# Kernel tuning notes

Measured on AMD Instinct MI355X. Metric: run time of the kernel, lower is better.

Reference implementation:

```python
import jax, jax.numpy as jnp
import numpy as np

KP_EXTENT = 1.2  # matches init_kwargs KP_extent


def setup_inputs() -> dict:
    key = jax.random.key(0)
    k1, k2, k3, k4, k5, k6 = jax.random.split(key, 6)
    N, M, H, K, CIN, COUT = 50000, 50000, 40, 15, 64, 128
    q_pts = jax.random.normal(k1, (N, 3), dtype=jnp.float32)
    s_pts = jax.random.normal(k2, (M, 3), dtype=jnp.float32)
    # indices in [0, M]; index M hits the padded shadow point / zero feature row
    neighb_inds = jax.random.randint(k3, (N, H), 0, M + 1)
    x = jax.random.normal(k4, (M, CIN), dtype=jnp.float32)
    # kernel point disposition in a sphere of given radius (values arbitrary for math check)
    kernel_points = jax.random.normal(k5, (K, 3), dtype=jnp.float32)
    weights = jax.random.normal(k6, (K, CIN, COUT), dtype=jnp.float32) * 0.05
    return {"q_pts": q_pts, "s_pts": s_pts, "neighb_inds": neighb_inds,
            "x": x, "kernel_points": kernel_points, "weights": weights}


def reference(q_pts, s_pts, neighb_inds, x, kernel_points, weights):
    # pad support points with a far-away shadow point (index M)
    shadow = jnp.full((1, s_pts.shape[1]), 1.0e6, dtype=s_pts.dtype)
    s_pad = jnp.concatenate([s_pts, shadow], axis=0)          # [M+1, 3]
    neighbors = s_pad[neighb_inds] - q_pts[:, None, :]        # [N, H, 3]

    # squared distances to kernel points via |n|^2 + |k|^2 - 2 n.k (avoids [N,H,K,3] tensor)
    n2 = jnp.sum(neighbors * neighbors, axis=-1)              # [N, H]
    k2 = jnp.sum(kernel_points * kernel_points, axis=-1)      # [K]
    cross = jnp.einsum('nhd,kd->nhk', neighbors, kernel_points)
    sq_distances = jnp.maximum(n2[:, :, None] + k2[None, None, :] - 2.0 * cross, 0.0)  # [N, H, K]

    # linear KP influence
    all_weights = jnp.clip(1.0 - jnp.sqrt(sq_distances) / KP_EXTENT, 0.0)  # [N, H, K]

    # pad features with a zero row for shadow neighbors
    x_pad = jnp.concatenate([x, jnp.zeros((1, x.shape[1]), dtype=x.dtype)], axis=0)  # [M+1, C]
    neighb_x = x_pad[neighb_inds]                             # [N, H, C]

    # weighted aggregation per kernel point, then per-kernel-point matmul and sum
    weighted_features = jnp.einsum('nhk,nhc->nkc', all_weights, neighb_x)  # [N, K, Cin]
    output_features = jnp.einsum('nkc,kco->no', weighted_features, weights)  # [N, Cout]

    # normalize by number of valid neighbors (feature-sum > 0 heuristic, as in source)
    neighbor_features_sum = jnp.sum(neighb_x, axis=-1)        # [N, H]
    neighbor_num = jnp.maximum(jnp.sum(neighbor_features_sum > 0.0, axis=-1), 1)  # [N]
    return output_features / neighbor_num[:, None].astype(output_features.dtype)
```

## Files before the change

kernel.cpp:

```cpp
#include <hip/hip_runtime.h>
#include <math.h>

typedef unsigned short ushort_t;
typedef __attribute__((ext_vector_type(8))) short bf16x8;
typedef __attribute__((ext_vector_type(4))) float f32x4;

constexpr int H    = 40;
constexpr int KKP  = 15;
constexpr int CIN  = 64;
constexpr int COUT = 128;
constexpr int QB   = 32;
constexpr int NT   = 512;
constexpr int NP   = QB * H;
constexpr int SWF  = 968;
constexpr int SWT  = 2056;
constexpr int CSTR = 48;
constexpr float INV_KPE = 1.0f / 1.2f;

constexpr int OFF_CIND = 61952;
constexpr int OFF_QCNT = 65152;
constexpr int OFF_CNT  = 65280;
constexpr int LDS_TOT  = 65408;
static_assert(LDS_TOT <= 65536, "LDS over 64KB static limit");

__device__ __forceinline__ ushort_t f2bf(float f) {
    union { float f; unsigned u; } v; v.f = f;
    unsigned r = v.u + 0x7FFFu + ((v.u >> 16) & 1u);
    return (ushort_t)(r >> 16);
}
__device__ __forceinline__ unsigned pk2(ushort_t a, ushort_t b) {
    return (unsigned)a | ((unsigned)b << 16);
}

__global__ __launch_bounds__(256) void prep_kernel(const float* __restrict__ x,
                                                   float* __restrict__ rowsum,
                                                   ushort_t* __restrict__ xb,
                                                   int M, int write_xb) {
    int row  = blockIdx.x * 4 + (threadIdx.x >> 6);
    int lane = threadIdx.x & 63;
    if (row >= M) return;
    float v = x[row * CIN + lane];
    if (write_xb) xb[row * CIN + lane] = f2bf(v);
    #pragma unroll
    for (int off = 32; off > 0; off >>= 1) v += __shfl_down(v, off, 64);
    if (lane == 0) rowsum[row] = v;
}

__global__ __launch_bounds__(256) void wprep_kernel(const float* __restrict__ wmat,
                                                    ushort_t* __restrict__ wb) {
    int t = blockIdx.x * 256 + threadIdx.x;
    if (t >= 30 * 8 * 64) return;
    int lane = t & 63;
    int ot   = (t >> 6) & 7;
    int jt   = t >> 9;
    int o  = ot * 16 + (lane & 15);
    int kb = jt * 32 + (lane >> 4) * 8;
    unsigned pk[4];
    #pragma unroll
    for (int r = 0; r < 4; ++r) {
        unsigned lo = f2bf(wmat[(kb + 2 * r) * COUT + o]);
        unsigned hi = f2bf(wmat[(kb + 2 * r + 1) * COUT + o]);
        pk[r] = lo | (hi << 16);
    }
    *(uint4*)&wb[(size_t)t * 8] = make_uint4(pk[0], pk[1], pk[2], pk[3]);
}

template<bool BF16X>
__global__ __launch_bounds__(NT, 4) void kpconv_main(
    const float* __restrict__ q_pts, const float* __restrict__ s_pts,
    const int*   __restrict__ nbinds, const float* __restrict__ xf,
    const ushort_t* __restrict__ xb,  const float* __restrict__ kp,
    const ushort_t* __restrict__ wb,  const float* __restrict__ rowsum,
    float* __restrict__ out, int N, int M)
{
    __shared__ __align__(16) unsigned char smem[LDS_TOT];
    ushort_t* const wT   = (ushort_t*)smem;
    ushort_t* const WF16 = (ushort_t*)smem;
    ushort_t* const cind = (ushort_t*)(smem + OFF_CIND);
    int* const qcnt = (int*)(smem + OFF_QCNT);
    int* const cnt  = (int*)(smem + OFF_CNT);

    const int tid = threadIdx.x;
    const int q0  = blockIdx.x * QB;

    for (int i = tid; i < 3855; i += NT)
        ((uint4*)wT)[i] = make_uint4(0, 0, 0, 0);
    if (tid < 200) ((uint4*)cind)[tid] = make_uint4(0, 0, 0, 0);
    if (tid < QB) { qcnt[tid] = 0; cnt[tid] = 0; }
    __syncthreads();

    for (int p = tid; p < NP; p += NT) {
        int q  = p / H;
        int h  = p - q * H;
        int gq  = q0 + q;
        int gqc = min(gq, N - 1);
        int ind = nbinds[gqc * H + h];
        bool shadow = (ind >= M);
        float nx = 0.f, ny = 0.f, nz = 0.f;
        if (!shadow) {
            nx = s_pts[ind * 3 + 0] - q_pts[gqc * 3 + 0];
            ny = s_pts[ind * 3 + 1] - q_pts[gqc * 3 + 1];
            nz = s_pts[ind * 3 + 2] - q_pts[gqc * 3 + 2];
            if (rowsum[ind] > 0.0f) atomicAdd(&cnt[q], 1);
        }
        float n2 = nx * nx + ny * ny + nz * nz;
        float w[KKP];
        float wmax = 0.f;
        #pragma unroll
        for (int k = 0; k < KKP; ++k) {
            float wv = 0.f;
            if (!shadow) {
                float kx = kp[k * 3 + 0], ky = kp[k * 3 + 1], kz = kp[k * 3 + 2];
                float k2 = kx * kx + ky * ky + kz * kz;
                float cross = nx * kx + ny * ky + nz * kz;
                float sq = fmaxf(n2 + k2 - 2.0f * cross, 0.0f);
                wv = fmaxf(1.0f - sqrtf(sq) * INV_KPE, 0.0f);
            }
            w[k] = wv;
            wmax = fmaxf(wmax, wv);
        }
        if (wmax > 0.f) {
            int slot = atomicAdd(&qcnt[q], 1);
            cind[q * CSTR + slot] = (ushort_t)ind;
            #pragma unroll
            for (int k = 0; k < KKP; ++k)
                wT[k * SWT + q * 64 + slot] = f2bf(w[k]);
        }
    }
    __syncthreads();

    const int wid  = tid >> 6;
    const int lane = tid & 63;
    const int l15  = lane & 15;
    const int kg   = lane >> 4;
    const int cg   = wid & 3;
    const int qh2  = wid >> 2;
    const int chan = cg * 16 + l15;
    const int arow = min(l15, 14);

    ushort_t dres[16][4];

    #define LOAD8(qq, base, arr)                                                  \
        {                                                                         \
            const int cb_ = (qq) * CSTR + (base);                                 \
            _Pragma("unroll")                                                     \
            for (int i = 0; i < 8; ++i) {                                         \
                int i0 = cind[cb_ + kg * 8 + i];                                  \
                if (BF16X) (arr)[i] = xb[((unsigned)i0 << 6) + chan];             \
                else       (arr)[i] = f2bf(xf[((unsigned)i0 << 6) + chan]);       \
            }                                                                     \
        }
    #define PACKB(arr, bv)                                                        \
        union { uint4 u; bf16x8 b; } bv;                                          \
        bv.u = make_uint4(pk2((arr)[0], (arr)[1]), pk2((arr)[2], (arr)[3]),       \
                          pk2((arr)[4], (arr)[5]), pk2((arr)[6], (arr)[7]));
    #define CONSUME1(qq, dd, arr)                                                 \
        {                                                                         \
            f32x4 acc = {0.f, 0.f, 0.f, 0.f};                                     \
            PACKB(arr, bv0)                                                       \
            bf16x8 a0 = *(const bf16x8*)&wT[arow * SWT + (qq) * 64 + kg * 8];     \
            acc = __builtin_amdgcn_mfma_f32_16x16x32_bf16(a0, bv0.b, acc, 0, 0, 0);\
            if (qcnt[qq] > 32) {                           \
                ushort_t ext[8];                                                  \
                LOAD8(qq, 32, ext);                  \
                PACKB(ext, bv1)                                                   \
                bf16x8 a1 = *(const bf16x8*)&wT[arow * SWT + (qq) * 64 + 32 + kg * 8];\
                acc = __builtin_amdgcn_mfma_f32_16x16x32_bf16(a1, bv1.b, acc, 0, 0, 0);\
            }                                                                     \
            _Pragma("unroll")                                                     \
            for (int reg = 0; reg < 4; ++reg) dres[dd][reg] = f2bf(acc[reg]);     \
        }

    #pragma unroll
    for (int t = 0; t < 2; ++t) {
        const int qb0 = (qh2 * 2 + t) * 8;
        ushort_t bA[4][8], bB[4][8];
        #pragma unroll
        for (int j = 0; j < 4; ++j) LOAD8(qb0 + j,     0, bA[j]);
        #pragma unroll
        for (int j = 0; j < 4; ++j) LOAD8(qb0 + 4 + j, 0, bB[j]);
        #pragma unroll
        for (int j = 0; j < 4; ++j) CONSUME1(qb0 + j,     t * 8 + j,     bA[j]);
        #pragma unroll
        for (int j = 0; j < 4; ++j) CONSUME1(qb0 + 4 + j, t * 8 + 4 + j, bB[j]);
    }
    #undef LOAD8
    #undef PACKB
    #undef CONSUME1
    __syncthreads();

    #pragma unroll
    for (int d = 0; d < 16; ++d) {
        int q = (qh2 * 2 + (d >> 3)) * 8 + (d & 7);
        #pragma unroll
        for (int reg = 0; reg < 4; ++reg) {
            int kpr = kg * 4 + reg;
            if (kpr < KKP)
                WF16[q * SWF + kpr * 64 + chan] = dres[d][reg];
        }
    }
    __syncthreads();

    {
        const int ot = wid;
        f32x4 c0 = {0.f, 0.f, 0.f, 0.f};
        f32x4 c1 = {0.f, 0.f, 0.f, 0.f};
        const ushort_t* wfrow0 = &WF16[l15 * SWF + kg * 8];
        const ushort_t* wfrow1 = &WF16[(16 + l15) * SWF + kg * 8];
        const ushort_t* bbase  = wb + ((size_t)(ot * 64 + lane)) * 8;

        bf16x8 rb0[6];
        #pragma unroll
        for (int i = 0; i < 6; ++i)
            rb0[i] = *(const bf16x8*)&bbase[(size_t)i * 4096];
        for (int m = 0; m < 5; ++m) {
            #pragma unroll
            for (int u = 0; u < 6; ++u) {
                int jt = m * 6 + u;
                bf16x8 a0 = *(const bf16x8*)&wfrow0[jt * 32];
                bf16x8 a1 = *(const bf16x8*)&wfrow1[jt * 32];
                c0 = __builtin_amdgcn_mfma_f32_16x16x32_bf16(a0, rb0[u], c0, 0, 0, 0);
                c1 = __builtin_amdgcn_mfma_f32_16x16x32_bf16(a1, rb0[u], c1, 0, 0, 0);
                if (m < 4)
                    rb0[u] = *(const bf16x8*)&bbase[(size_t)(jt + 6) * 4096];
            }
        }

        int col = ot * 16 + l15;
        #pragma unroll
        for (int reg = 0; reg < 4; ++reg) {
            int row = kg * 4 + reg;
            int gqa = q0 + row;
            if (gqa < N) {
                float inv = 1.0f / (float)max(cnt[row], 1);
                out[(size_t)gqa * COUT + col] = c0[reg] * inv;
            }
            int gqb = q0 + 16 + row;
            if (gqb < N) {
                float inv = 1.0f / (float)max(cnt[16 + row], 1);
                out[(size_t)gqb * COUT + col] = c1[reg] * inv;
            }
        }
    }
}

extern "C" void kernel_launch(void* const* d_in, const int* in_sizes, int n_in,
                              void* d_out, int out_size, void* d_ws, size_t ws_size,
                              hipStream_t stream) {
    const float* q_pts  = (const float*)d_in[0];
    const float* s_pts  = (const float*)d_in[1];
    const int*   nbinds = (const int*)d_in[2];
    const float* x      = (const float*)d_in[3];
    const float* kp     = (const float*)d_in[4];
    const float* wmat   = (const float*)d_in[5];
    float* out = (float*)d_out;
    int N = in_sizes[0] / 3;
    int M = in_sizes[1] / 3;

    size_t    off_wb = ((size_t)M * 4 + 255) & ~(size_t)255;
    size_t    off_xb = (off_wb + 245760 + 255) & ~(size_t)255;
    size_t    need   = off_xb + (size_t)M * CIN * 2;
    float*    rowsum = (float*)d_ws;
    ushort_t* wb     = (ushort_t*)((char*)d_ws + off_wb);
    ushort_t* xb     = (ushort_t*)((char*)d_ws + off_xb);
    bool use_bf16x = (ws_size >= need) && (M < 65536);

    prep_kernel<<<(M + 3) / 4, 256, 0, stream>>>(x, rowsum, xb, M, use_bf16x ? 1 : 0);
    wprep_kernel<<<60, 256, 0, stream>>>(wmat, wb);
    int mb = (N + QB - 1) / QB;
    if (use_bf16x)
        kpconv_main<true><<<mb, NT, 0, stream>>>(q_pts, s_pts, nbinds, x, xb, kp,
                                                 wb, rowsum, out, N, M);
    else
        kpconv_main<false><<<mb, NT, 0, stream>>>(q_pts, s_pts, nbinds, x, xb, kp,
                                                  wb, rowsum, out, N, M);
}
```

Measured before the change: 93.53 us.

## Give each wave private query slices to replace block barriers with wave-local fences

Each wave now owns four queries and handles their zeroing, neighbor weight computation, compaction and the first-stage MFMA over all 64 channels itself. Because LDS data is only touched by the owning wave in these phases, the two block-wide barriers are replaced with an lgkmcnt wait plus a scheduling barrier. Compacted neighbor indices are read as one 16-byte vector instead of eight scalar LDS reads, and feature loads are software-pipelined across queries. Per-wave load balance now depends on each query's neighbor count, and each wave holds more registers for the four channel tiles.

```diff
diff --git a/kernel.cpp b/kernel.cpp
--- a/kernel.cpp
+++ b/kernel.cpp
@@ -11,7 +11,6 @@
 constexpr int COUT = 128;
 constexpr int QB   = 32;
 constexpr int NT   = 512;
-constexpr int NP   = QB * H;
 constexpr int SWF  = 968;
 constexpr int SWT  = 2056;
 constexpr int CSTR = 48;
@@ -23,6 +22,8 @@
 constexpr int LDS_TOT  = 65408;
 static_assert(LDS_TOT <= 65536, "LDS over 64KB static limit");
 
+#define MFMA32(a, b, c) __builtin_amdgcn_mfma_f32_16x16x32_bf16(a, b, c, 0, 0, 0)
+
 __device__ __forceinline__ ushort_t f2bf(float f) {
     union { float f; unsigned u; } v; v.f = f;
     unsigned r = v.u + 0x7FFFu + ((v.u >> 16) & 1u);
@@ -30,6 +31,10 @@
 }
 __device__ __forceinline__ unsigned pk2(ushort_t a, ushort_t b) {
     return (unsigned)a | ((unsigned)b << 16);
+}
+__device__ __forceinline__ void lds_fence() {
+    asm volatile("s_waitcnt lgkmcnt(0)" ::: "memory");
+    __builtin_amdgcn_sched_barrier(0);
 }
 
 __global__ __launch_bounds__(256) void prep_kernel(const float* __restrict__ x,
@@ -80,123 +85,169 @@
     int* const qcnt = (int*)(smem + OFF_QCNT);
     int* const cnt  = (int*)(smem + OFF_CNT);
 
-    const int tid = threadIdx.x;
-    const int q0  = blockIdx.x * QB;
-
-    for (int i = tid; i < 3855; i += NT)
-        ((uint4*)wT)[i] = make_uint4(0, 0, 0, 0);
-    if (tid < 200) ((uint4*)cind)[tid] = make_uint4(0, 0, 0, 0);
-    if (tid < QB) { qcnt[tid] = 0; cnt[tid] = 0; }
-    __syncthreads();
-
-    for (int p = tid; p < NP; p += NT) {
-        int q  = p / H;
-        int h  = p - q * H;
-        int gq  = q0 + q;
-        int gqc = min(gq, N - 1);
-        int ind = nbinds[gqc * H + h];
-        bool shadow = (ind >= M);
-        float nx = 0.f, ny = 0.f, nz = 0.f;
-        if (!shadow) {
-            nx = s_pts[ind * 3 + 0] - q_pts[gqc * 3 + 0];
-            ny = s_pts[ind * 3 + 1] - q_pts[gqc * 3 + 1];
-            nz = s_pts[ind * 3 + 2] - q_pts[gqc * 3 + 2];
-            if (rowsum[ind] > 0.0f) atomicAdd(&cnt[q], 1);
-        }
-        float n2 = nx * nx + ny * ny + nz * nz;
-        float w[KKP];
-        float wmax = 0.f;
-        #pragma unroll
-        for (int k = 0; k < KKP; ++k) {
-            float wv = 0.f;
-            if (!shadow) {
-                float kx = kp[k * 3 + 0], ky = kp[k * 3 + 1], kz = kp[k * 3 + 2];
-                float k2 = kx * kx + ky * ky + kz * kz;
-                float cross = nx * kx + ny * ky + nz * kz;
-                float sq = fmaxf(n2 + k2 - 2.0f * cross, 0.0f);
-                wv = fmaxf(1.0f - sqrtf(sq) * INV_KPE, 0.0f);
-            }
-            w[k] = wv;
-            wmax = fmaxf(wmax, wv);
-        }
-        if (wmax > 0.f) {
-            int slot = atomicAdd(&qcnt[q], 1);
-            cind[q * CSTR + slot] = (ushort_t)ind;
-            #pragma unroll
-            for (int k = 0; k < KKP; ++k)
-                wT[k * SWT + q * 64 + slot] = f2bf(w[k]);
-        }
-    }
-    __syncthreads();
-
+    const int tid  = threadIdx.x;
     const int wid  = tid >> 6;
     const int lane = tid & 63;
+    const int q0   = blockIdx.x * QB;
+    const int wq0  = wid * 4;
+
+    const uint4 z4 = make_uint4(0, 0, 0, 0);
+    for (int j = lane; j < 480; j += 64) {
+        int r = j >> 5, c = j & 31;
+        *(uint4*)&wT[r * SWT + wq0 * 64 + c * 8] = z4;
+    }
+    if (lane < 24) ((uint4*)&cind[wq0 * CSTR])[lane] = z4;
+    if (lane < 4) { qcnt[wq0 + lane] = 0; cnt[wq0 + lane] = 0; }
+    lds_fence();
+
+    #pragma unroll
+    for (int i = 0; i < 3; ++i) {
+        int pp = i * 64 + lane;
+        if (pp < 160) {
+            int qd = pp / H;
+            int q  = wq0 + qd;
+            int h  = pp - qd * H;
+            int gq  = q0 + q;
+            int gqc = min(gq, N - 1);
+            int ind = nbinds[gqc * H + h];
+            bool shadow = (ind >= M);
+            float nx = 0.f, ny = 0.f, nz = 0.f;
+            if (!shadow) {
+                nx = s_pts[ind * 3 + 0] - q_pts[gqc * 3 + 0];
+                ny = s_pts[ind * 3 + 1] - q_pts[gqc * 3 + 1];
+                nz = s_pts[ind * 3 + 2] - q_pts[gqc * 3 + 2];
+                if (rowsum[ind] > 0.0f) atomicAdd(&cnt[q], 1);
+            }
+            float n2 = nx * nx + ny * ny + nz * nz;
+            float w[KKP];
+            float wmax = 0.f;
+            #pragma unroll
+            for (int k = 0; k < KKP; ++k) {
+                float wv = 0.f;
+                if (!shadow) {
+                    float kx = kp[k * 3 + 0], ky = kp[k * 3 + 1], kz = kp[k * 3 + 2];
+                    float k2 = kx * kx + ky * ky + kz * kz;
+                    float cross = nx * kx + ny * ky + nz * kz;
+                    float sq = fmaxf(n2 + k2 - 2.0f * cross, 0.0f);
+                    wv = fmaxf(1.0f - sqrtf(sq) * INV_KPE, 0.0f);
+                }
+                w[k] = wv;
+                wmax = fmaxf(wmax, wv);
+            }
+            if (wmax > 0.f) {
+                int slot = atomicAdd(&qcnt[q], 1);
+                cind[q * CSTR + slot] = (ushort_t)ind;
+                #pragma unroll
+                for (int k = 0; k < KKP; ++k)
+                    wT[k * SWT + q * 64 + slot] = f2bf(w[k]);
+            }
+        }
+    }
+    lds_fence();
+
     const int l15  = lane & 15;
     const int kg   = lane >> 4;
-    const int cg   = wid & 3;
-    const int qh2  = wid >> 2;
-    const int chan = cg * 16 + l15;
     const int arow = min(l15, 14);
 
-    ushort_t dres[16][4];
-
-    #define LOAD8(qq, base, arr)                                                  \
-        {                                                                         \
-            const int cb_ = (qq) * CSTR + (base);                                 \
-            _Pragma("unroll")                                                     \
-            for (int i = 0; i < 8; ++i) {                                         \
-                int i0 = cind[cb_ + kg * 8 + i];                                  \
-                if (BF16X) (arr)[i] = xb[((unsigned)i0 << 6) + chan];             \
-                else       (arr)[i] = f2bf(xf[((unsigned)i0 << 6) + chan]);       \
-            }                                                                     \
-        }
-    #define PACKB(arr, bv)                                                        \
-        union { uint4 u; bf16x8 b; } bv;                                          \
-        bv.u = make_uint4(pk2((arr)[0], (arr)[1]), pk2((arr)[2], (arr)[3]),       \
+    unsigned dpk[4][4][2];
+
+    #define GETIDX(qq, base, idx)                                             \
+        {                                                                     \
+            int ofs_ = (base) + kg * 8;                                       \
+            if (ofs_ + 7 >= CSTR) ofs_ = 0;                                   \
+            uint4 cv = *(const uint4*)&cind[(qq) * CSTR + ofs_];              \
+            idx[0] = (ushort_t)(cv.x & 0xffff); idx[1] = (ushort_t)(cv.x >> 16);\
+            idx[2] = (ushort_t)(cv.y & 0xffff); idx[3] = (ushort_t)(cv.y >> 16);\
+            idx[4] = (ushort_t)(cv.z & 0xffff); idx[5] = (ushort_t)(cv.z >> 16);\
+            idx[6] = (ushort_t)(cv.w & 0xffff); idx[7] = (ushort_t)(cv.w >> 16);\
+        }
+    #define LOAD32(qq, bank)                                                  \
+        {                                                                     \
+            ushort_t idx[8];                                                  \
+            GETIDX(qq, 0, idx)                                                \
+            _Pragma("unroll")                                                 \
+            for (int i = 0; i < 8; ++i) {                                     \
+                unsigned ba = ((unsigned)idx[i] << 6) + l15;                  \
+                _Pragma("unroll")                                             \
+                for (int ct = 0; ct < 4; ++ct) {                              \
+                    if (BF16X) bank[ct][i] = xb[ba + ct * 16];                \
+                    else       bank[ct][i] = f2bf(xf[ba + ct * 16]);          \
+                }                                                             \
+            }                                                                 \
+        }
+    #define PACKB(arr, bv)                                                    \
+        union { uint4 u; bf16x8 b; } bv;                                      \
+        bv.u = make_uint4(pk2((arr)[0], (arr)[1]), pk2((arr)[2], (arr)[3]),   \
                           pk2((arr)[4], (arr)[5]), pk2((arr)[6], (arr)[7]));
-    #define CONSUME1(qq, dd, arr)                                                 \
-        {                                                                         \
-            f32x4 acc = {0.f, 0.f, 0.f, 0.f};                                     \
-            PACKB(arr, bv0)                                                       \
-            bf16x8 a0 = *(const bf16x8*)&wT[arow * SWT + (qq) * 64 + kg * 8];     \
-            acc = __builtin_amdgcn_mfma_f32_16x16x32_bf16(a0, bv0.b, acc, 0, 0, 0);\
-            if (qcnt[qq] > 32) {                           \
-                ushort_t ext[8];                                                  \
-                LOAD8(qq, 32, ext);                  \
-                PACKB(ext, bv1)                                                   \
+    #define CHUNK2(ct, accv)                                                  \
+        {                                                                     \
+            ushort_t e[8];                                                    \
+            _Pragma("unroll")                                                 \
+            for (int i = 0; i < 8; ++i) {                                     \
+                unsigned ba = ((unsigned)idx2[i] << 6) + l15 + (ct) * 16;     \
+                e[i] = BF16X ? xb[ba] : f2bf(xf[ba]);                         \
+            }                                                                 \
+            PACKB(e, bv_)                                                     \
+            accv = MFMA32(a1, bv_.b, accv);                                   \
+        }
+    #define CONSUME_Q(qq, qi, bank)                                           \
+        {                                                                     \
+            bf16x8 a0 = *(const bf16x8*)&wT[arow * SWT + (qq) * 64 + kg * 8]; \
+            f32x4 z_ = {0.f, 0.f, 0.f, 0.f};                                  \
+            f32x4 ac0 = z_, ac1 = z_, ac2 = z_, ac3 = z_;                     \
+            { PACKB(bank[0], v0) ac0 = MFMA32(a0, v0.b, ac0); }               \
+            { PACKB(bank[1], v1) ac1 = MFMA32(a0, v1.b, ac1); }               \
+            { PACKB(bank[2], v2) ac2 = MFMA32(a0, v2.b, ac2); }               \
+            { PACKB(bank[3], v3) ac3 = MFMA32(a0, v3.b, ac3); }               \
+            if (qcnt[qq] > 32) {                       \
+                ushort_t idx2[8];                                             \
+                GETIDX(qq, 32, idx2)                                          \
                 bf16x8 a1 = *(const bf16x8*)&wT[arow * SWT + (qq) * 64 + 32 + kg * 8];\
-                acc = __builtin_amdgcn_mfma_f32_16x16x32_bf16(a1, bv1.b, acc, 0, 0, 0);\
-            }                                                                     \
-            _Pragma("unroll")                                                     \
-            for (int reg = 0; reg < 4; ++reg) dres[dd][reg] = f2bf(acc[reg]);     \
-        }
+                CHUNK2(0, ac0) CHUNK2(1, ac1) CHUNK2(2, ac2) CHUNK2(3, ac3)   \
+            }                                                                 \
+            dpk[qi][0][0] = pk2(f2bf(ac0[0]), f2bf(ac0[1]));                  \
+            dpk[qi][0][1] = pk2(f2bf(ac0[2]), f2bf(ac0[3]));                  \
+            dpk[qi][1][0] = pk2(f2bf(ac1[0]), f2bf(ac1[1]));                  \
+            dpk[qi][1][1] = pk2(f2bf(ac1[2]), f2bf(ac1[3]));                  \
+            dpk[qi][2][0] = pk2(f2bf(ac2[0]), f2bf(ac2[1]));                  \
+            dpk[qi][2][1] = pk2(f2bf(ac2[2]), f2bf(ac2[3]));                  \
+            dpk[qi][3][0] = pk2(f2bf(ac3[0]), f2bf(ac3[1]));                  \
+            dpk[qi][3][1] = pk2(f2bf(ac3[2]), f2bf(ac3[3]));                  \
+        }
+
+    {
+        ushort_t bA[4][8], bB[4][8];
+        LOAD32(wq0 + 0, bA)
+        LOAD32(wq0 + 1, bB)
+        CONSUME_Q(wq0 + 0, 0, bA)
+        LOAD32(wq0 + 2, bA)
+        CONSUME_Q(wq0 + 1, 1, bB)
+        LOAD32(wq0 + 3, bB)
+        CONSUME_Q(wq0 + 2, 2, bA)
+        CONSUME_Q(wq0 + 3, 3, bB)
+    }
+    #undef GETIDX
+    #undef LOAD32
+    #undef PACKB
+    #undef CHUNK2
+    #undef CONSUME_Q
+
+    __syncthreads();
 
     #pragma unroll
-    for (int t = 0; t < 2; ++t) {
-        const int qb0 = (qh2 * 2 + t) * 8;
-        ushort_t bA[4][8], bB[4][8];
+    for (int qi = 0; qi < 4; ++qi) {
+        int q = wq0 + qi;
         #pragma unroll
-        for (int j = 0; j < 4; ++j) LOAD8(qb0 + j,     0, bA[j]);
-        #pragma unroll
-        for (int j = 0; j < 4; ++j) LOAD8(qb0 + 4 + j, 0, bB[j]);
-        #pragma unroll
-        for (int j = 0; j < 4; ++j) CONSUME1(qb0 + j,     t * 8 + j,     bA[j]);
-        #pragma unroll
-        for (int j = 0; j < 4; ++j) CONSUME1(qb0 + 4 + j, t * 8 + 4 + j, bB[j]);
-    }
-    #undef LOAD8
-    #undef PACKB
-    #undef CONSUME1
-    __syncthreads();
-
-    #pragma unroll
-    for (int d = 0; d < 16; ++d) {
-        int q = (qh2 * 2 + (d >> 3)) * 8 + (d & 7);
-        #pragma unroll
-        for (int reg = 0; reg < 4; ++reg) {
-            int kpr = kg * 4 + reg;
-            if (kpr < KKP)
-                WF16[q * SWF + kpr * 64 + chan] = dres[d][reg];
+        for (int ct = 0; ct < 4; ++ct) {
+            int col = ct * 16 + l15;
+            #pragma unroll
+            for (int pr = 0; pr < 2; ++pr) {
+                unsigned d = dpk[qi][ct][pr];
+                int k0 = kg * 4 + pr * 2;
+                WF16[q * SWF + k0 * 64 + col] = (ushort_t)(d & 0xffff);
+                if (k0 + 1 < KKP)
+                    WF16[q * SWF + (k0 + 1) * 64 + col] = (ushort_t)(d >> 16);
+            }
         }
     }
     __syncthreads();
@@ -219,8 +270,8 @@
                 int jt = m * 6 + u;
                 bf16x8 a0 = *(const bf16x8*)&wfrow0[jt * 32];
                 bf16x8 a1 = *(const bf16x8*)&wfrow1[jt * 32];
-                c0 = __builtin_amdgcn_mfma_f32_16x16x32_bf16(a0, rb0[u], c0, 0, 0, 0);
-                c1 = __builtin_amdgcn_mfma_f32_16x16x32_bf16(a1, rb0[u], c1, 0, 0, 0);
+                c0 = MFMA32(a0, rb0[u], c0);
+                c1 = MFMA32(a1, rb0[u], c1);
                 if (m < 4)
                     rb0[u] = *(const bf16x8*)&bbase[(size_t)(jt + 6) * 4096];
             }
```

After: 92.95 us. Within noise of the previous version (-0.6%).
